# Kernel optimization log

Hardware: AMD Instinct MI355X
Metric: run time of the kernel (lower is better)

The kernel has to match this reference:

```python
import jax, jax.numpy as jnp
import numpy as np


def _maxpool2(x):
    # x: [B, C, H, W] -> [B, C, H//2, W//2], 2x2 max pool stride 2
    B, C, H, W = x.shape
    return x.reshape(B, C, H // 2, 2, W // 2, 2).max(axis=(3, 5))


def setup_inputs() -> dict:
    key = jax.random.key(0)
    ks = jax.random.split(key, 6)
    B, C, H, W = 16, 128, 64, 64
    x = jax.random.normal(ks[0], (B, C, H, W), dtype=jnp.float32)
    wq = jax.random.normal(ks[1], (C // 8, C), dtype=jnp.float32) * 0.05
    wk = jax.random.normal(ks[2], (C // 8, C), dtype=jnp.float32) * 0.05
    wv = jax.random.normal(ks[3], (C // 2, C), dtype=jnp.float32) * 0.05
    wo = jax.random.normal(ks[4], (C, C // 2), dtype=jnp.float32) * 0.05
    gamma = jax.random.uniform(ks[5], (1,), dtype=jnp.float32)
    return {"x": x, "wq": wq, "wk": wk, "wv": wv, "wo": wo, "gamma": gamma}


def reference(x, wq, wk, wv, wo, gamma):
    B, C, H, W = x.shape
    N = H * W
    M = N // 4
    # 1x1 convs are channel contractions
    q = jnp.einsum('oc,bchw->bohw', wq, x)              # [B, C/8, H, W]
    k = _maxpool2(jnp.einsum('oc,bchw->bohw', wk, x))   # [B, C/8, H/2, W/2]
    v = _maxpool2(jnp.einsum('oc,bchw->bohw', wv, x))   # [B, C/2, H/2, W/2]
    q = q.reshape(B, C // 8, N)
    k = k.reshape(B, C // 8, M)
    v = v.reshape(B, C // 2, M)
    attn = jax.nn.softmax(jnp.einsum('bcn,bcm->bnm', q, k), axis=-1)  # [B, N, M]
    o = jnp.einsum('bcm,bnm->bcn', v, attn).reshape(B, C // 2, H, W)
    o = jnp.einsum('oc,bchw->bohw', wo, o)              # [B, C, H, W]
    return gamma[0] * o + x
```

## Files before the change

### kernel.cpp

```cpp
#include <hip/hip_runtime.h>


#define LOG2E 1.4426950408889634f

typedef __attribute__((ext_vector_type(8)))  short bf16x8;
typedef __attribute__((ext_vector_type(16))) float f32x16;
typedef unsigned long long ull;

static __device__ __forceinline__ unsigned cvt_pk_bf16(float a, float b) {
  unsigned r;
  asm("v_cvt_pk_bf16_f32 %0, %1, %2" : "=v"(r) : "v"(a), "v"(b));
  return r;
}
static __device__ __forceinline__ void perm32swap(unsigned& a, unsigned& b) {
  asm volatile("v_permlane32_swap_b32 %0, %1" : "+v"(a), "+v"(b));
}
static __device__ __forceinline__ float fexp2(float x) {
  float r; asm("v_exp_f32 %0, %1" : "=v"(r) : "v"(x)); return r;
}
static __device__ __forceinline__ bf16x8 pack4(unsigned u0, unsigned u1,
                                               unsigned u2, unsigned u3) {
  union { bf16x8 v; unsigned u[4]; } r;
  r.u[0] = u0; r.u[1] = u1; r.u[2] = u2; r.u[3] = u3;
  return r.v;
}
static __device__ __forceinline__ bf16x8 pack2ull(ull a, ull b) {
  union { bf16x8 v; ull u[2]; } r;
  r.u[0] = a; r.u[1] = b;
  return r.v;
}
static __device__ __forceinline__ short f2bf(float f) {
  unsigned u = __float_as_uint(f);
  u = (u + 0x7FFFu + ((u >> 16) & 1u)) >> 16;
  return (short)u;
}
static __device__ __forceinline__ int swzj(int j) {
  return j ^ ((j >> 2) & 7) ^ (((j >> 6) & 1) << 2);
}
#define FK(V, K) ((K) == 0 ? (V).x : (K) == 1 ? (V).y : (K) == 2 ? (V).z : (V).w)

#define WSTRIDE 136

__global__ __launch_bounds__(256) void proj_kernel(
    const float* __restrict__ x, const float* __restrict__ wq,
    const float* __restrict__ wk, const float* __restrict__ wv,
    short* __restrict__ qT, short* __restrict__ kT, short* __restrict__ vT)
{
  __shared__ short x_s[16 * 1024];
  __shared__ short w_s[96 * WSTRIDE];
  __shared__ short v_s[2048];

  const int b = blockIdx.y, t = threadIdx.x;
  const int wid = t >> 6, lane = t & 63;
  const int l31 = lane & 31, hi = lane >> 5;
  const int r = blockIdx.x;
  const float* xb = x + (size_t)b * 128 * 4096 + r * 128;

  const int j4  = (t & 31) * 4;
  const int c00 = (t >> 5) * 8;
  #pragma unroll
  for (int R = 0; R < 2; ++R) {
    float4 f[8];
    #pragma unroll
    for (int i = 0; i < 8; ++i)
      f[i] = *(const float4*)(xb + (size_t)(c00 + i + R * 64) * 4096 + j4);
    const int g = (t >> 5) + R * 8;
    #pragma unroll
    for (int k = 0; k < 4; ++k) {
      const bf16x8 frag = pack4(
          cvt_pk_bf16(FK(f[0], k), FK(f[1], k)),
          cvt_pk_bf16(FK(f[2], k), FK(f[3], k)),
          cvt_pk_bf16(FK(f[4], k), FK(f[5], k)),
          cvt_pk_bf16(FK(f[6], k), FK(f[7], k)));
      *(bf16x8*)&x_s[g * 1024 + swzj(j4 + k) * 8] = frag;
    }
  }

  #pragma unroll
  for (int kk = 0; kk < 12; ++kk) {
    const int idx = t + kk * 256;
    const int row = idx >> 5, c4 = (idx & 31) << 2;
    const float* src = (row < 16) ? (wq + row * 128 + c4)
                     : (row < 32) ? (wk + (row - 16) * 128 + c4)
                                  : (wv + (row - 32) * 128 + c4);
    const float4 f = *(const float4*)src;
    const ull v = ((ull)cvt_pk_bf16(f.z, f.w) << 32) | (ull)cvt_pk_bf16(f.x, f.y);
    *(ull*)&w_s[row * WSTRIDE + c4] = v;
  }
  __syncthreads();

  const int p_local = wid * 32 + l31;
  const int q2l = p_local >> 2, rr = p_local & 3;
  const int jl = (rr >> 1) * 64 + q2l * 2 + (rr & 1);
  const int p = r * 128 + p_local;

  bf16x8 xf[8];
  #pragma unroll
  for (int cc = 0; cc < 8; ++cc)
    xf[cc] = *(const bf16x8*)&x_s[(cc * 2 + hi) * 1024 + swzj(jl) * 8];

  f32x16 acc0, acc1, acc2;
  #pragma unroll
  for (int j = 0; j < 16; ++j) { acc0[j] = 0.f; acc1[j] = 0.f; acc2[j] = 0.f; }

  #pragma unroll
  for (int cc = 0; cc < 8; ++cc) {
    const int off = cc * 16 + hi * 8;
    const bf16x8 a0 = *(const bf16x8*)&w_s[l31 * WSTRIDE + off];
    const bf16x8 a1 = *(const bf16x8*)&w_s[(32 + l31) * WSTRIDE + off];
    const bf16x8 a2 = *(const bf16x8*)&w_s[(64 + l31) * WSTRIDE + off];
    acc0 = __builtin_amdgcn_mfma_f32_32x32x16_bf16(a0, xf[cc], acc0, 0, 0, 0);
    acc1 = __builtin_amdgcn_mfma_f32_32x32x16_bf16(a1, xf[cc], acc1, 0, 0, 0);
    acc2 = __builtin_amdgcn_mfma_f32_32x32x16_bf16(a2, xf[cc], acc2, 0, 0, 0);
  }

  {
    unsigned u0 = cvt_pk_bf16(acc0[0] * LOG2E, acc0[1] * LOG2E);
    unsigned u1 = cvt_pk_bf16(acc0[2] * LOG2E, acc0[3] * LOG2E);
    unsigned u2 = cvt_pk_bf16(acc0[4] * LOG2E, acc0[5] * LOG2E);
    unsigned u3 = cvt_pk_bf16(acc0[6] * LOG2E, acc0[7] * LOG2E);
    perm32swap(u0, u2); perm32swap(u1, u3);
    *(bf16x8*)(qT + ((size_t)b * 4096 + p) * 16 + hi * 8) = pack4(u0, u1, u2, u3);
  }

  {
    float pk[8];
    #pragma unroll
    for (int rg = 8; rg < 16; ++rg) {
      float m = acc0[rg];
      m = fmaxf(m, __shfl_xor(m, 1));
      m = fmaxf(m, __shfl_xor(m, 2));
      pk[rg - 8] = m;
    }
    unsigned u0 = cvt_pk_bf16(pk[0], pk[1]), u1 = cvt_pk_bf16(pk[2], pk[3]);
    unsigned u2 = cvt_pk_bf16(pk[4], pk[5]), u3 = cvt_pk_bf16(pk[6], pk[7]);
    perm32swap(u0, u2); perm32swap(u1, u3);
    if ((l31 & 3) == 0)
      *(bf16x8*)(kT + ((size_t)b * 1024 + (p >> 2)) * 16 + hi * 8) =
          pack4(u0, u1, u2, u3);
  }

  {
    float pv1[16], pv2[16];
    #pragma unroll
    for (int rg = 0; rg < 16; ++rg) {
      float m1 = acc1[rg], m2 = acc2[rg];
      m1 = fmaxf(m1, __shfl_xor(m1, 1)); m1 = fmaxf(m1, __shfl_xor(m1, 2));
      m2 = fmaxf(m2, __shfl_xor(m2, 1)); m2 = fmaxf(m2, __shfl_xor(m2, 2));
      pv1[rg] = m1; pv2[rg] = m2;
    }
    if ((l31 & 3) == 0) {
      const int q2p = wid * 8 + (l31 >> 2);
      const int ks = q2p >> 4, mm = q2p & 15;
      #pragma unroll
      for (int rg = 0; rg < 16; ++rg) {
        const int c2 = (rg & 3) + 8 * (rg >> 2) + 4 * hi;
        v_s[ks * 1024 + c2 * 16 + mm]        = f2bf(pv1[rg]);
        v_s[ks * 1024 + (32 + c2) * 16 + mm] = f2bf(pv2[rg]);
      }
    }
  }
  __syncthreads();
  *(bf16x8*)(vT + (size_t)b * 65536 + r * 2048 + t * 8) =
      *(const bf16x8*)&v_s[t * 8];
}

#define WOSTRIDE 68

__global__ __launch_bounds__(256) void attn_kernel(
    const short* __restrict__ qT, const short* __restrict__ kT,
    const short* __restrict__ vT, const float* __restrict__ wo,
    const float* __restrict__ x, const float* __restrict__ gamma,
    float* __restrict__ out)
{
  __shared__ float obuf[2][2][64][18];
  __shared__ float lbuf[2][2][64];
  __shared__ short wo_s[128 * WOSTRIDE];

  const int t = threadIdx.x;
  const int wid = t >> 6, lane = t & 63;
  const int l31 = lane & 31, hi = lane >> 5;
  const int qhalf = wid >> 1, mhalf = wid & 1;

  const int wg = blockIdx.x;
  const int sw = (wg & 7) * 128 + (wg >> 3);
  const int b = sw >> 6;
  const int p = (sw & 63) * 64 + qhalf * 32 + l31;

  #pragma unroll
  for (int kk = 0; kk < 8; ++kk) {
    const int idx = t + kk * 256;
    const int row = idx >> 4, c4 = (idx & 15) << 2;
    const float4 f = *(const float4*)(wo + row * 64 + c4);
    const ull v = ((ull)cvt_pk_bf16(f.z, f.w) << 32) | (ull)cvt_pk_bf16(f.x, f.y);
    *(ull*)&wo_s[row * WOSTRIDE + c4] = v;
  }

  const short* kTb = kT + (size_t)b * 1024 * 16;
  const short* vb  = vT + (size_t)b * 65536;
  const bf16x8 qf = *(const bf16x8*)(qT + ((size_t)b * 4096 + p) * 16 + hi * 8);

  f32x16 z, o0, o1;
  #pragma unroll
  for (int j = 0; j < 16; ++j) { z[j] = 0.f; o0[j] = 0.f; o1[j] = 0.f; }
  float l = 0.f;

  const int mtbase = mhalf * 16;

  bf16x8 kfA, v00A, v01A, v10A, v11A;
  bf16x8 kfB, v00B, v01B, v10B, v11B;

#define LOADT(S, MT) do {                                                    \
    const int mt_ = (MT);                                                    \
    kf##S  = *(const bf16x8*)(kTb + (size_t)(mt_ * 32 + l31) * 16 + hi * 8); \
    const short* tb_ = vb + (size_t)mt_ * 2048 + l31 * 16 + hi * 8;          \
    v00##S = *(const bf16x8*)(tb_);                                          \
    v10##S = *(const bf16x8*)(tb_ + 512);                                    \
    v01##S = *(const bf16x8*)(tb_ + 1024);                                   \
    v11##S = *(const bf16x8*)(tb_ + 1536); } while (0)

#define COMP(S) do {                                                         \
    f32x16 s = __builtin_amdgcn_mfma_f32_32x32x16_bf16(kf##S, qf, z, 0, 0, 0);\
    float pe[16];                                                            \
    _Pragma("unroll")                                                        \
    for (int j = 0; j < 16; ++j) pe[j] = fexp2(s[j]);                        \
    l += ((pe[0]+pe[1])+(pe[2]+pe[3])) + ((pe[4]+pe[5])+(pe[6]+pe[7]))       \
       + ((pe[8]+pe[9])+(pe[10]+pe[11])) + ((pe[12]+pe[13])+(pe[14]+pe[15]));\
    unsigned a0 = cvt_pk_bf16(pe[0], pe[1]),  a1 = cvt_pk_bf16(pe[2], pe[3]);\
    unsigned a2 = cvt_pk_bf16(pe[4], pe[5]),  a3 = cvt_pk_bf16(pe[6], pe[7]);\
    perm32swap(a0, a2); perm32swap(a1, a3);                                  \
    const bf16x8 P0 = pack4(a0, a1, a2, a3);                                 \
    unsigned c0 = cvt_pk_bf16(pe[8], pe[9]),   c1 = cvt_pk_bf16(pe[10], pe[11]);\
    unsigned c2 = cvt_pk_bf16(pe[12], pe[13]), c3 = cvt_pk_bf16(pe[14], pe[15]);\
    perm32swap(c0, c2); perm32swap(c1, c3);                                  \
    const bf16x8 P1 = pack4(c0, c1, c2, c3);                                 \
    o0 = __builtin_amdgcn_mfma_f32_32x32x16_bf16(v00##S, P0, o0, 0, 0, 0);   \
    o0 = __builtin_amdgcn_mfma_f32_32x32x16_bf16(v01##S, P1, o0, 0, 0, 0);   \
    o1 = __builtin_amdgcn_mfma_f32_32x32x16_bf16(v10##S, P0, o1, 0, 0, 0);   \
    o1 = __builtin_amdgcn_mfma_f32_32x32x16_bf16(v11##S, P1, o1, 0, 0, 0); } while (0)

  LOADT(A, mtbase);
  #pragma unroll 1
  for (int mt = 0; mt < 16; mt += 2) {
    LOADT(B, mtbase + mt + 1);
    __builtin_amdgcn_s_setprio(1);
    COMP(A);
    __builtin_amdgcn_s_setprio(0);
    const int mn = (mt + 2 < 16) ? mtbase + mt + 2 : mtbase;
    LOADT(A, mn);
    __builtin_amdgcn_s_setprio(1);
    COMP(B);
    __builtin_amdgcn_s_setprio(0);
  }
#undef LOADT
#undef COMP

  l += __shfl_xor(l, 32);
  float* mybuf = &obuf[qhalf][mhalf][lane][0];
  const float* pbuf = &obuf[qhalf][mhalf ^ 1][lane][0];

  #pragma unroll
  for (int j = 0; j < 16; ++j) mybuf[j] = o0[j];
  lbuf[qhalf][mhalf][lane] = l;
  __syncthreads();
  #pragma unroll
  for (int j = 0; j < 16; ++j) o0[j] += pbuf[j];
  l += lbuf[qhalf][mhalf ^ 1][lane];
  __syncthreads();
  #pragma unroll
  for (int j = 0; j < 16; ++j) mybuf[j] = o1[j];
  __syncthreads();
  #pragma unroll
  for (int j = 0; j < 16; ++j) o1[j] += pbuf[j];

  const float inv = 1.0f / l;

  float on[32];
  #pragma unroll
  for (int j = 0; j < 16; ++j) { on[j] = o0[j] * inv; on[16 + j] = o1[j] * inv; }

  bf16x8 ofr[4];
  #pragma unroll
  for (int ck = 0; ck < 4; ++ck) {
    const int base = (ck >> 1) * 16 + (ck & 1) * 8;
    unsigned a0 = cvt_pk_bf16(on[base + 0], on[base + 1]);
    unsigned a1 = cvt_pk_bf16(on[base + 2], on[base + 3]);
    unsigned a2 = cvt_pk_bf16(on[base + 4], on[base + 5]);
    unsigned a3 = cvt_pk_bf16(on[base + 6], on[base + 7]);
    perm32swap(a0, a2); perm32swap(a1, a3);
    ofr[ck] = pack4(a0, a1, a2, a3);
  }

  const int q2 = p >> 2, rr = p & 3;
  const int nsp = ((((q2 >> 5) << 1) | (rr >> 1)) << 6) | (((q2 & 31) << 1) | (rr & 1));
  const float g = gamma[0];
  const float* xb = x + (size_t)b * 128 * 4096 + nsp;
  float* ob = out + (size_t)b * 128 * 4096 + nsp;

  #pragma unroll 1
  for (int ci = 0; ci < 2; ++ci) {
    const int cot = mhalf * 2 + ci;
    f32x16 acc;
    #pragma unroll
    for (int j = 0; j < 16; ++j) acc[j] = 0.f;
    #pragma unroll
    for (int ck = 0; ck < 4; ++ck) {
      const short* pw = &wo_s[(cot * 32 + l31) * WOSTRIDE + ck * 16 + hi * 8];
      const bf16x8 wf = pack2ull(*(const ull*)pw, *(const ull*)(pw + 4));
      acc = __builtin_amdgcn_mfma_f32_32x32x16_bf16(wf, ofr[ck], acc, 0, 0, 0);
    }
    #pragma unroll
    for (int rg = 0; rg < 16; ++rg) {
      const int co = cot * 32 + (rg & 3) + 8 * (rg >> 2) + 4 * hi;
      ob[(size_t)co * 4096] = g * acc[rg] + xb[(size_t)co * 4096];
    }
  }
}

extern "C" void kernel_launch(void* const* d_in, const int* in_sizes, int n_in,
                              void* d_out, int out_size, void* d_ws, size_t ws_size,
                              hipStream_t stream) {
  const float* x     = (const float*)d_in[0];
  const float* wq    = (const float*)d_in[1];
  const float* wk    = (const float*)d_in[2];
  const float* wv    = (const float*)d_in[3];
  const float* wo    = (const float*)d_in[4];
  const float* gamma = (const float*)d_in[5];
  float* out = (float*)d_out;

  short* ws = (short*)d_ws;
  short* qT = ws;
  short* kT = ws + 1048576;
  short* vT = ws + 1310720;

  proj_kernel<<<dim3(32, 16), 256, 0, stream>>>(x, wq, wk, wv, qT, kT, vT);
  attn_kernel<<<dim3(1024), 256, 0, stream>>>(qT, kT, vT, wo, x, gamma, out);
}
```

Baseline: 120.0 us.

## Share V tiles via LDS across four query waves and halve proj LDS

The attention kernel now gives each workgroup 128 queries, one 32-query tile per wave, and each wave walks all 32 key tiles. This replaces the old split of key tiles across wave pairs, which needed an LDS reduction at the end. V tiles are loaded cooperatively into a swizzled, double-buffered LDS area, so each tile is shared by the four waves instead of every wave reading it from global memory, and the grid is halved. The projection kernel processes channels in two halves through a half-size x_s buffer to cut LDS use and possibly raise occupancy. The cost is two barriers per iteration in the attention loop and an extra barrier pair in the projection kernel.

```diff
diff --git a/kernel.cpp b/kernel.cpp
--- a/kernel.cpp
+++ b/kernel.cpp
@@ -46,7 +46,7 @@
     const float* __restrict__ wk, const float* __restrict__ wv,
     short* __restrict__ qT, short* __restrict__ kT, short* __restrict__ vT)
 {
-  __shared__ short x_s[16 * 1024];
+  __shared__ short x_s[8 * 1024];
   __shared__ short w_s[96 * WSTRIDE];
   __shared__ short v_s[2048];
 
@@ -58,23 +58,13 @@
 
   const int j4  = (t & 31) * 4;
   const int c00 = (t >> 5) * 8;
-  #pragma unroll
-  for (int R = 0; R < 2; ++R) {
-    float4 f[8];
-    #pragma unroll
-    for (int i = 0; i < 8; ++i)
-      f[i] = *(const float4*)(xb + (size_t)(c00 + i + R * 64) * 4096 + j4);
-    const int g = (t >> 5) + R * 8;
-    #pragma unroll
-    for (int k = 0; k < 4; ++k) {
-      const bf16x8 frag = pack4(
-          cvt_pk_bf16(FK(f[0], k), FK(f[1], k)),
-          cvt_pk_bf16(FK(f[2], k), FK(f[3], k)),
-          cvt_pk_bf16(FK(f[4], k), FK(f[5], k)),
-          cvt_pk_bf16(FK(f[6], k), FK(f[7], k)));
-      *(bf16x8*)&x_s[g * 1024 + swzj(j4 + k) * 8] = frag;
-    }
-  }
+  float4 f0_[8], f1_[8];
+  #pragma unroll
+  for (int i = 0; i < 8; ++i)
+    f0_[i] = *(const float4*)(xb + (size_t)(c00 + i) * 4096 + j4);
+  #pragma unroll
+  for (int i = 0; i < 8; ++i)
+    f1_[i] = *(const float4*)(xb + (size_t)(c00 + i + 64) * 4096 + j4);
 
   #pragma unroll
   for (int kk = 0; kk < 12; ++kk) {
@@ -87,6 +77,17 @@
     const ull v = ((ull)cvt_pk_bf16(f.z, f.w) << 32) | (ull)cvt_pk_bf16(f.x, f.y);
     *(ull*)&w_s[row * WSTRIDE + c4] = v;
   }
+
+  const int g = t >> 5;
+  #pragma unroll
+  for (int k = 0; k < 4; ++k) {
+    const bf16x8 frag = pack4(
+        cvt_pk_bf16(FK(f0_[0], k), FK(f0_[1], k)),
+        cvt_pk_bf16(FK(f0_[2], k), FK(f0_[3], k)),
+        cvt_pk_bf16(FK(f0_[4], k), FK(f0_[5], k)),
+        cvt_pk_bf16(FK(f0_[6], k), FK(f0_[7], k)));
+    *(bf16x8*)&x_s[g * 1024 + swzj(j4 + k) * 8] = frag;
+  }
   __syncthreads();
 
   const int p_local = wid * 32 + l31;
@@ -94,24 +95,44 @@
   const int jl = (rr >> 1) * 64 + q2l * 2 + (rr & 1);
   const int p = r * 128 + p_local;
 
-  bf16x8 xf[8];
-  #pragma unroll
-  for (int cc = 0; cc < 8; ++cc)
-    xf[cc] = *(const bf16x8*)&x_s[(cc * 2 + hi) * 1024 + swzj(jl) * 8];
-
   f32x16 acc0, acc1, acc2;
   #pragma unroll
   for (int j = 0; j < 16; ++j) { acc0[j] = 0.f; acc1[j] = 0.f; acc2[j] = 0.f; }
 
   #pragma unroll
-  for (int cc = 0; cc < 8; ++cc) {
+  for (int cc = 0; cc < 4; ++cc) {
+    const bf16x8 xf = *(const bf16x8*)&x_s[(cc * 2 + hi) * 1024 + swzj(jl) * 8];
     const int off = cc * 16 + hi * 8;
     const bf16x8 a0 = *(const bf16x8*)&w_s[l31 * WSTRIDE + off];
     const bf16x8 a1 = *(const bf16x8*)&w_s[(32 + l31) * WSTRIDE + off];
     const bf16x8 a2 = *(const bf16x8*)&w_s[(64 + l31) * WSTRIDE + off];
-    acc0 = __builtin_amdgcn_mfma_f32_32x32x16_bf16(a0, xf[cc], acc0, 0, 0, 0);
-    acc1 = __builtin_amdgcn_mfma_f32_32x32x16_bf16(a1, xf[cc], acc1, 0, 0, 0);
-    acc2 = __builtin_amdgcn_mfma_f32_32x32x16_bf16(a2, xf[cc], acc2, 0, 0, 0);
+    acc0 = __builtin_amdgcn_mfma_f32_32x32x16_bf16(a0, xf, acc0, 0, 0, 0);
+    acc1 = __builtin_amdgcn_mfma_f32_32x32x16_bf16(a1, xf, acc1, 0, 0, 0);
+    acc2 = __builtin_amdgcn_mfma_f32_32x32x16_bf16(a2, xf, acc2, 0, 0, 0);
+  }
+  __syncthreads();
+
+  #pragma unroll
+  for (int k = 0; k < 4; ++k) {
+    const bf16x8 frag = pack4(
+        cvt_pk_bf16(FK(f1_[0], k), FK(f1_[1], k)),
+        cvt_pk_bf16(FK(f1_[2], k), FK(f1_[3], k)),
+        cvt_pk_bf16(FK(f1_[4], k), FK(f1_[5], k)),
+        cvt_pk_bf16(FK(f1_[6], k), FK(f1_[7], k)));
+    *(bf16x8*)&x_s[g * 1024 + swzj(j4 + k) * 8] = frag;
+  }
+  __syncthreads();
+
+  #pragma unroll
+  for (int cc = 4; cc < 8; ++cc) {
+    const bf16x8 xf = *(const bf16x8*)&x_s[((cc - 4) * 2 + hi) * 1024 + swzj(jl) * 8];
+    const int off = cc * 16 + hi * 8;
+    const bf16x8 a0 = *(const bf16x8*)&w_s[l31 * WSTRIDE + off];
+    const bf16x8 a1 = *(const bf16x8*)&w_s[(32 + l31) * WSTRIDE + off];
+    const bf16x8 a2 = *(const bf16x8*)&w_s[(64 + l31) * WSTRIDE + off];
+    acc0 = __builtin_amdgcn_mfma_f32_32x32x16_bf16(a0, xf, acc0, 0, 0, 0);
+    acc1 = __builtin_amdgcn_mfma_f32_32x32x16_bf16(a1, xf, acc1, 0, 0, 0);
+    acc2 = __builtin_amdgcn_mfma_f32_32x32x16_bf16(a2, xf, acc2, 0, 0, 0);
   }
 
   {
@@ -173,19 +194,17 @@
     const float* __restrict__ x, const float* __restrict__ gamma,
     float* __restrict__ out)
 {
-  __shared__ float obuf[2][2][64][18];
-  __shared__ float lbuf[2][2][64];
   __shared__ short wo_s[128 * WOSTRIDE];
+  __shared__ short v_lds[2 * 2048];
 
   const int t = threadIdx.x;
   const int wid = t >> 6, lane = t & 63;
   const int l31 = lane & 31, hi = lane >> 5;
-  const int qhalf = wid >> 1, mhalf = wid & 1;
 
   const int wg = blockIdx.x;
-  const int sw = (wg & 7) * 128 + (wg >> 3);
-  const int b = sw >> 6;
-  const int p = (sw & 63) * 64 + qhalf * 32 + l31;
+  const int sw = (wg & 7) * 64 + (wg >> 3);
+  const int b = sw >> 5;
+  const int p = (sw & 31) * 128 + wid * 32 + l31;
 
   #pragma unroll
   for (int kk = 0; kk < 8; ++kk) {
@@ -200,27 +219,23 @@
   const short* vb  = vT + (size_t)b * 65536;
   const bf16x8 qf = *(const bf16x8*)(qT + ((size_t)b * 4096 + p) * 16 + hi * 8);
 
+  const int wdst  = (t * 16) ^ (((t >> 1) & 7) << 4);
+  const int rbase = (l31 * 32 + hi * 16) ^ ((l31 & 7) << 4);
+
   f32x16 z, o0, o1;
   #pragma unroll
   for (int j = 0; j < 16; ++j) { z[j] = 0.f; o0[j] = 0.f; o1[j] = 0.f; }
   float l = 0.f;
 
-  const int mtbase = mhalf * 16;
-
-  bf16x8 kfA, v00A, v01A, v10A, v11A;
-  bf16x8 kfB, v00B, v01B, v10B, v11B;
-
-#define LOADT(S, MT) do {                                                    \
-    const int mt_ = (MT);                                                    \
-    kf##S  = *(const bf16x8*)(kTb + (size_t)(mt_ * 32 + l31) * 16 + hi * 8); \
-    const short* tb_ = vb + (size_t)mt_ * 2048 + l31 * 16 + hi * 8;          \
-    v00##S = *(const bf16x8*)(tb_);                                          \
-    v10##S = *(const bf16x8*)(tb_ + 512);                                    \
-    v01##S = *(const bf16x8*)(tb_ + 1024);                                   \
-    v11##S = *(const bf16x8*)(tb_ + 1536); } while (0)
-
-#define COMP(S) do {                                                         \
+  bf16x8 kfA, kfB, vregA, vregB;
+
+#define COMP(S, BUF) do {                                                    \
     f32x16 s = __builtin_amdgcn_mfma_f32_32x32x16_bf16(kf##S, qf, z, 0, 0, 0);\
+    const char* vp_ = (const char*)v_lds + (BUF) * 4096 + rbase;             \
+    const bf16x8 w00 = *(const bf16x8*)(vp_);                                \
+    const bf16x8 w10 = *(const bf16x8*)(vp_ + 1024);                         \
+    const bf16x8 w01 = *(const bf16x8*)(vp_ + 2048);                         \
+    const bf16x8 w11 = *(const bf16x8*)(vp_ + 3072);                         \
     float pe[16];                                                            \
     _Pragma("unroll")                                                        \
     for (int j = 0; j < 16; ++j) pe[j] = fexp2(s[j]);                        \
@@ -234,45 +249,37 @@
     unsigned c2 = cvt_pk_bf16(pe[12], pe[13]), c3 = cvt_pk_bf16(pe[14], pe[15]);\
     perm32swap(c0, c2); perm32swap(c1, c3);                                  \
     const bf16x8 P1 = pack4(c0, c1, c2, c3);                                 \
-    o0 = __builtin_amdgcn_mfma_f32_32x32x16_bf16(v00##S, P0, o0, 0, 0, 0);   \
-    o0 = __builtin_amdgcn_mfma_f32_32x32x16_bf16(v01##S, P1, o0, 0, 0, 0);   \
-    o1 = __builtin_amdgcn_mfma_f32_32x32x16_bf16(v10##S, P0, o1, 0, 0, 0);   \
-    o1 = __builtin_amdgcn_mfma_f32_32x32x16_bf16(v11##S, P1, o1, 0, 0, 0); } while (0)
-
-  LOADT(A, mtbase);
+    __builtin_amdgcn_s_setprio(1);                                           \
+    o0 = __builtin_amdgcn_mfma_f32_32x32x16_bf16(w00, P0, o0, 0, 0, 0);      \
+    o0 = __builtin_amdgcn_mfma_f32_32x32x16_bf16(w01, P1, o0, 0, 0, 0);      \
+    o1 = __builtin_amdgcn_mfma_f32_32x32x16_bf16(w10, P0, o1, 0, 0, 0);      \
+    o1 = __builtin_amdgcn_mfma_f32_32x32x16_bf16(w11, P1, o1, 0, 0, 0);      \
+    __builtin_amdgcn_s_setprio(0); } while (0)
+
+  vregA = *(const bf16x8*)(vb + t * 8);
+  kfA   = *(const bf16x8*)(kTb + (size_t)l31 * 16 + hi * 8);
+  *(bf16x8*)((char*)v_lds + wdst) = vregA;
+  __syncthreads();
+
   #pragma unroll 1
-  for (int mt = 0; mt < 16; mt += 2) {
-    LOADT(B, mtbase + mt + 1);
-    __builtin_amdgcn_s_setprio(1);
-    COMP(A);
-    __builtin_amdgcn_s_setprio(0);
-    const int mn = (mt + 2 < 16) ? mtbase + mt + 2 : mtbase;
-    LOADT(A, mn);
-    __builtin_amdgcn_s_setprio(1);
-    COMP(B);
-    __builtin_amdgcn_s_setprio(0);
-  }
-#undef LOADT
+  for (int mt = 0; mt < 32; mt += 2) {
+    vregB = *(const bf16x8*)(vb + (size_t)(mt + 1) * 2048 + t * 8);
+    kfB   = *(const bf16x8*)(kTb + (size_t)((mt + 1) * 32 + l31) * 16 + hi * 8);
+    COMP(A, 0);
+    *(bf16x8*)((char*)v_lds + 4096 + wdst) = vregB;
+    __syncthreads();
+    if (mt < 30) {
+      vregA = *(const bf16x8*)(vb + (size_t)(mt + 2) * 2048 + t * 8);
+      kfA   = *(const bf16x8*)(kTb + (size_t)((mt + 2) * 32 + l31) * 16 + hi * 8);
+    }
+    COMP(B, 1);
+    if (mt < 30)
+      *(bf16x8*)((char*)v_lds + wdst) = vregA;
+    __syncthreads();
+  }
 #undef COMP
 
   l += __shfl_xor(l, 32);
-  float* mybuf = &obuf[qhalf][mhalf][lane][0];
-  const float* pbuf = &obuf[qhalf][mhalf ^ 1][lane][0];
-
-  #pragma unroll
-  for (int j = 0; j < 16; ++j) mybuf[j] = o0[j];
-  lbuf[qhalf][mhalf][lane] = l;
-  __syncthreads();
-  #pragma unroll
-  for (int j = 0; j < 16; ++j) o0[j] += pbuf[j];
-  l += lbuf[qhalf][mhalf ^ 1][lane];
-  __syncthreads();
-  #pragma unroll
-  for (int j = 0; j < 16; ++j) mybuf[j] = o1[j];
-  __syncthreads();
-  #pragma unroll
-  for (int j = 0; j < 16; ++j) o1[j] += pbuf[j];
-
   const float inv = 1.0f / l;
 
   float on[32];
@@ -298,8 +305,7 @@
   float* ob = out + (size_t)b * 128 * 4096 + nsp;
 
   #pragma unroll 1
-  for (int ci = 0; ci < 2; ++ci) {
-    const int cot = mhalf * 2 + ci;
+  for (int cot = 0; cot < 4; ++cot) {
     f32x16 acc;
     #pragma unroll
     for (int j = 0; j < 16; ++j) acc[j] = 0.f;
@@ -334,5 +340,5 @@
   short* vT = ws + 1310720;
 
   proj_kernel<<<dim3(32, 16), 256, 0, stream>>>(x, wq, wk, wv, qT, kT, vT);
-  attn_kernel<<<dim3(1024), 256, 0, stream>>>(qT, kT, vT, wo, x, gamma, out);
-}
+  attn_kernel<<<dim3(512), 256, 0, stream>>>(qT, kT, vT, wo, x, gamma, out);
+}
```

Measured after the change: 125.8 us. +4.9%, slower.
